# Performance work log

Hardware: AMD Instinct MI355X
Metric: run time of the kernel (lower is better)

## Reference

```python
import jax, jax.numpy as jnp
import numpy as np

MAX_DISP = 24  # matches init_kwargs


def setup_inputs() -> dict:
    key = jax.random.key(0)
    k1, k2 = jax.random.split(key)
    B, H, W, C = 2, 256, 256, 16
    left = jax.random.normal(k1, (B, H, W, C), dtype=jnp.float32)
    right = jax.random.normal(k2, (B, H, W, C), dtype=jnp.float32)
    return {"left": left, "right": right}


def reference(left, right):
    # left/right: [B, H, W, C]. Builds concat cost volume [B, 2*max_disp, H, W, 2C].
    # For disparity i in [-max_disp, max_disp): out[d, :, w] pairs left[w] with
    # right[w - i]; positions where w - i falls outside [0, W) are zero-padded
    # (both the left and right halves, matching tf.pad of the concatenated slice).
    W = left.shape[2]
    disps = jnp.arange(-MAX_DISP, MAX_DISP)              # [2D]
    idx = jnp.arange(W)[None, :] - disps[:, None]        # [2D, W] source col in right
    valid = (idx >= 0) & (idx < W)                       # [2D, W]
    idx_c = jnp.clip(idx, 0, W - 1)
    mask = valid[None, None, :, :, None].astype(left.dtype)  # [1,1,2D,W,1]
    r = right[:, :, idx_c, :] * mask                     # [B,H,2D,W,C]
    l = left[:, :, None, :, :] * mask                    # [B,H,2D,W,C]
    vol = jnp.concatenate([l, r], axis=-1)               # [B,H,2D,W,2C]
    return jnp.transpose(vol, (0, 2, 1, 3, 4))           # [B,2D,H,W,2C]
```

## Files before the change

kernel.cpp:

```cpp
#include <hip/hip_runtime.h>


#define MAXD 24
#define ND   48
#define HH   256
#define WW   256

__global__ __launch_bounds__(1024) void FeatureVolume_68762426409246_kernel(
    const float4* __restrict__ left,
    const float4* __restrict__ right,
    float4* __restrict__ out) {
    __shared__ float4 lds[2 * WW * 4];

    const unsigned int bh  = blockIdx.x;
    const unsigned int b   = bh >> 8;
    const unsigned int tid = threadIdx.x;

    const unsigned int row_base = bh * (WW * 4);
    lds[tid]          = left [row_base + tid];
    lds[WW * 4 + tid] = right[row_base + tid];
    __syncthreads();

    const unsigned int out_base = (b * (ND * HH) + (bh & 255u)) * (WW * 8);

    const unsigned int total = ND * WW * 8;
    for (unsigned int idx = tid; idx < total; idx += 1024) {
        unsigned int c4 = idx & 7u;
        unsigned int w  = (idx >> 3) & 255u;
        unsigned int d  = idx >> 11;

        int src_w  = (int)w - ((int)d - MAXD);
        bool valid = ((unsigned)src_w < (unsigned)WW);

        int col_r = min(max(src_w, 0), WW - 1);
        unsigned int col  = (c4 < 4u) ? w : (unsigned)col_r;
        unsigned int half = (c4 < 4u) ? 0u : (unsigned)(WW * 4);

        float4 v = lds[half + col * 4u + (c4 & 3u)];
        float  m = valid ? 1.0f : 0.0f;

        out[out_base + d * (HH * WW * 8) + (idx & 2047u)] =
            make_float4(v.x * m, v.y * m, v.z * m, v.w * m);
    }
}

extern "C" void kernel_launch(void* const* d_in, const int* in_sizes, int n_in,
                              void* d_out, int out_size, void* d_ws, size_t ws_size,
                              hipStream_t stream) {
    const float4* left  = (const float4*)d_in[0];
    const float4* right = (const float4*)d_in[1];
    float4* out = (float4*)d_out;

    FeatureVolume_68762426409246_kernel<<<2 * HH, 1024, 0, stream>>>(
        left, right, out);
}
```

Measured before the change: 152.4 us.

## Scatter each input float4 to all disparity slices instead of gathering via LDS

```diff
diff --git a/kernel.cpp b/kernel.cpp
--- a/kernel.cpp
+++ b/kernel.cpp
@@ -5,42 +5,45 @@
 #define ND   48
 #define HH   256
 #define WW   256
+#define SLICE_F4 (HH * WW * 8)
 
-__global__ __launch_bounds__(1024) void FeatureVolume_68762426409246_kernel(
+__global__ __launch_bounds__(256) void FeatureVolume_68762426409246_kernel(
     const float4* __restrict__ left,
     const float4* __restrict__ right,
     float4* __restrict__ out) {
-    __shared__ float4 lds[2 * WW * 4];
+    const unsigned int g = blockIdx.x * 256u + threadIdx.x;
 
-    const unsigned int bh  = blockIdx.x;
-    const unsigned int b   = bh >> 8;
-    const unsigned int tid = threadIdx.x;
+    const float4 L = left[g];
+    const float4 R = right[g];
 
-    const unsigned int row_base = bh * (WW * 4);
-    lds[tid]          = left [row_base + tid];
-    lds[WW * 4 + tid] = right[row_base + tid];
-    __syncthreads();
+    const unsigned int c4q = g & 3u;
+    const unsigned int w   = (g >> 2) & 255u;
+    const unsigned int h   = (g >> 10) & 255u;
+    const unsigned int b   = g >> 18;
 
-    const unsigned int out_base = (b * (ND * HH) + (bh & 255u)) * (WW * 8);
+    unsigned long long baseA =
+        (unsigned long long)(b * ND) * SLICE_F4 +
+        (unsigned long long)((h * WW + w) * 8u + c4q);
+    float4* pA = out + baseA;
+    float4* pC = pA + (-(int)MAXD * 8 + 4);
 
-    const unsigned int total = ND * WW * 8;
-    for (unsigned int idx = tid; idx < total; idx += 1024) {
-        unsigned int c4 = idx & 7u;
-        unsigned int w  = (idx >> 3) & 255u;
-        unsigned int d  = idx >> 11;
+    const float4 Z = make_float4(0.f, 0.f, 0.f, 0.f);
 
-        int src_w  = (int)w - ((int)d - MAXD);
-        bool valid = ((unsigned)src_w < (unsigned)WW);
+    int vA = (int)w + MAXD;
+    int vC = (int)w - MAXD;
 
-        int col_r = min(max(src_w, 0), WW - 1);
-        unsigned int col  = (c4 < 4u) ? w : (unsigned)col_r;
-        unsigned int half = (c4 < 4u) ? 0u : (unsigned)(WW * 4);
+    #pragma unroll 4
+    for (int d = 0; d < ND; ++d) {
+        const bool valid = ((unsigned int)vA < (unsigned int)WW);
 
-        float4 v = lds[half + col * 4u + (c4 & 3u)];
-        float  m = valid ? 1.0f : 0.0f;
+        pA[0] = valid ? L : Z;
+        if (!valid) pA[4] = Z;
+        if ((unsigned int)vC < (unsigned int)WW) pC[0] = R;
 
-        out[out_base + d * (HH * WW * 8) + (idx & 2047u)] =
-            make_float4(v.x * m, v.y * m, v.z * m, v.w * m);
+        pA += SLICE_F4;
+        pC += SLICE_F4 + 8;
+        vA -= 1;
+        vC += 1;
     }
 }
 
@@ -51,6 +54,6 @@
     const float4* right = (const float4*)d_in[1];
     float4* out = (float4*)d_out;
 
-    FeatureVolume_68762426409246_kernel<<<2 * HH, 1024, 0, stream>>>(
+    FeatureVolume_68762426409246_kernel<<<2048, 256, 0, stream>>>(
         left, right, out);
 }
```

Measured after the change: 275.4 us. 80.6% more time.

## Keep left features in registers and batch four disparities per loop iteration

Applied to the files above, without the earlier changes.

```diff
diff --git a/kernel.cpp b/kernel.cpp
--- a/kernel.cpp
+++ b/kernel.cpp
@@ -5,42 +5,54 @@
 #define ND   48
 #define HH   256
 #define WW   256
+#define SLICE 524288u
 
 __global__ __launch_bounds__(1024) void FeatureVolume_68762426409246_kernel(
     const float4* __restrict__ left,
     const float4* __restrict__ right,
     float4* __restrict__ out) {
-    __shared__ float4 lds[2 * WW * 4];
+    __shared__ float4 rlds[WW * 4];
 
     const unsigned int bh  = blockIdx.x;
     const unsigned int b   = bh >> 8;
-    const unsigned int tid = threadIdx.x;
+    const unsigned int t   = threadIdx.x;
+    const unsigned int c4  = t & 7u;
+    const unsigned int wlo = t >> 3;
+    const unsigned int row = bh << 10;
 
-    const unsigned int row_base = bh * (WW * 4);
-    lds[tid]          = left [row_base + tid];
-    lds[WW * 4 + tid] = right[row_base + tid];
+    rlds[t] = right[row + t];
+
+    const unsigned int lbase = row + (wlo << 2) + (c4 & 3u);
+    const float4 L0 = left[lbase];
+    const float4 L1 = left[lbase + 512u];
     __syncthreads();
 
-    const unsigned int out_base = (b * (ND * HH) + (bh & 255u)) * (WW * 8);
+    const bool   isL = (c4 < 4u);
+    const float4 Z   = make_float4(0.f, 0.f, 0.f, 0.f);
 
-    const unsigned int total = ND * WW * 8;
-    for (unsigned int idx = tid; idx < total; idx += 1024) {
-        unsigned int c4 = idx & 7u;
-        unsigned int w  = (idx >> 3) & 255u;
-        unsigned int d  = idx >> 11;
+    float4* o0 = out + (((unsigned long long)(b * ND * HH + (bh & 255u))) << 11) + t;
 
-        int src_w  = (int)w - ((int)d - MAXD);
-        bool valid = ((unsigned)src_w < (unsigned)WW);
-
-        int col_r = min(max(src_w, 0), WW - 1);
-        unsigned int col  = (c4 < 4u) ? w : (unsigned)col_r;
-        unsigned int half = (c4 < 4u) ? 0u : (unsigned)(WW * 4);
-
-        float4 v = lds[half + col * 4u + (c4 & 3u)];
-        float  m = valid ? 1.0f : 0.0f;
-
-        out[out_base + d * (HH * WW * 8) + (idx & 2047u)] =
-            make_float4(v.x * m, v.y * m, v.z * m, v.w * m);
+    for (int d = 0; d < ND; d += 4) {
+        float4 v[4][2];
+        #pragma unroll
+        for (int k = 0; k < 4; ++k) {
+            const int s0 = (int)wlo + MAXD - (d + k);
+            const int s1 = s0 + 128;
+            const int c0 = min(max(s0, 0), WW - 1);
+            const int c1 = min(max(s1, 0), WW - 1);
+            const float4 r0 = rlds[(c0 << 2) + (int)(c4 & 3u)];
+            const float4 r1 = rlds[(c1 << 2) + (int)(c4 & 3u)];
+            const float4 a0 = isL ? L0 : r0;
+            const float4 a1 = isL ? L1 : r1;
+            v[k][0] = ((unsigned)s0 < (unsigned)WW) ? a0 : Z;
+            v[k][1] = ((unsigned)s1 < (unsigned)WW) ? a1 : Z;
+        }
+        #pragma unroll
+        for (int k = 0; k < 4; ++k) {
+            float4* p = o0 + (unsigned)(d + k) * SLICE;
+            p[0]    = v[k][0];
+            p[1024] = v[k][1];
+        }
     }
 }
 
```

Result: slower. 479.1 us (+214.3%).

## Split work by disparity and row chunk with double-buffered LDS row prefetch

Applied to the files above, without the earlier changes.

```diff
diff --git a/kernel.cpp b/kernel.cpp
--- a/kernel.cpp
+++ b/kernel.cpp
@@ -5,42 +5,72 @@
 #define ND   48
 #define HH   256
 #define WW   256
+#define HC   16
+#define ROW_F4 1024
+#define OUT_ROW_F4 2048
+#define SLICE_F4 (HH * OUT_ROW_F4)
 
 __global__ __launch_bounds__(1024) void FeatureVolume_68762426409246_kernel(
     const float4* __restrict__ left,
     const float4* __restrict__ right,
     float4* __restrict__ out) {
-    __shared__ float4 lds[2 * WW * 4];
+    __shared__ float4 buf[2][2 * ROW_F4];
 
-    const unsigned int bh  = blockIdx.x;
-    const unsigned int b   = bh >> 8;
-    const unsigned int tid = threadIdx.x;
+    const unsigned bid = blockIdx.x;
+    const unsigned hc  = bid & 15u;
+    const unsigned bd  = bid >> 4;
+    const unsigned b   = (bd >= ND) ? 1u : 0u;
+    const unsigned d   = bd - b * ND;
+    const unsigned t   = threadIdx.x;
 
-    const unsigned int row_base = bh * (WW * 4);
-    lds[tid]          = left [row_base + tid];
-    lds[WW * 4 + tid] = right[row_base + tid];
+    const unsigned h0 = hc * HC;
+    const float4* lrow = left  + (size_t)(b * HH + h0) * ROW_F4;
+    const float4* rrow = right + (size_t)(b * HH + h0) * ROW_F4;
+
+    {
+        float4 lv = lrow[t];
+        float4 rv = rrow[t];
+        buf[0][t]          = lv;
+        buf[0][ROW_F4 + t] = rv;
+    }
     __syncthreads();
 
-    const unsigned int out_base = (b * (ND * HH) + (bh & 255u)) * (WW * 8);
+    const unsigned c4 = t & 7u;
+    const unsigned w  = t >> 3;
+    const bool isL = (c4 < 4u);
+    const int s0 = (int)w + MAXD - (int)d;
+    const int s1 = s0 + 128;
+    const bool val0 = ((unsigned)s0 < (unsigned)WW);
+    const bool val1 = ((unsigned)s1 < (unsigned)WW);
+    const unsigned cr0 = (unsigned)min(max(s0, 0), WW - 1);
+    const unsigned cr1 = (unsigned)min(max(s1, 0), WW - 1);
+    const unsigned a0 = isL ? (w * 4u + c4)
+                            : (ROW_F4 + cr0 * 4u + (c4 - 4u));
+    const unsigned a1 = isL ? ((w + 128u) * 4u + c4)
+                            : (ROW_F4 + cr1 * 4u + (c4 - 4u));
+    const float4 Z = make_float4(0.f, 0.f, 0.f, 0.f);
 
-    const unsigned int total = ND * WW * 8;
-    for (unsigned int idx = tid; idx < total; idx += 1024) {
-        unsigned int c4 = idx & 7u;
-        unsigned int w  = (idx >> 3) & 255u;
-        unsigned int d  = idx >> 11;
+    float4* op = out + (size_t)bd * SLICE_F4 + (size_t)h0 * OUT_ROW_F4 + t;
 
-        int src_w  = (int)w - ((int)d - MAXD);
-        bool valid = ((unsigned)src_w < (unsigned)WW);
-
-        int col_r = min(max(src_w, 0), WW - 1);
-        unsigned int col  = (c4 < 4u) ? w : (unsigned)col_r;
-        unsigned int half = (c4 < 4u) ? 0u : (unsigned)(WW * 4);
-
-        float4 v = lds[half + col * 4u + (c4 & 3u)];
-        float  m = valid ? 1.0f : 0.0f;
-
-        out[out_base + d * (HH * WW * 8) + (idx & 2047u)] =
-            make_float4(v.x * m, v.y * m, v.z * m, v.w * m);
+    unsigned pp = 0;
+    for (int i = 0; i < HC; ++i) {
+        float4 lv, rv;
+        const bool more = (i + 1 < HC);
+        if (more) {
+            lv = lrow[(size_t)(i + 1) * ROW_F4 + t];
+            rv = rrow[(size_t)(i + 1) * ROW_F4 + t];
+        }
+        float4 x0 = buf[pp][a0];
+        float4 x1 = buf[pp][a1];
+        op[0]    = val0 ? x0 : Z;
+        op[1024] = val1 ? x1 : Z;
+        if (more) {
+            buf[pp ^ 1][t]          = lv;
+            buf[pp ^ 1][ROW_F4 + t] = rv;
+        }
+        __syncthreads();
+        pp ^= 1;
+        op += OUT_ROW_F4;
     }
 }
 
@@ -51,6 +81,6 @@
     const float4* right = (const float4*)d_in[1];
     float4* out = (float4*)d_out;
 
-    FeatureVolume_68762426409246_kernel<<<2 * HH, 1024, 0, stream>>>(
+    FeatureVolume_68762426409246_kernel<<<2 * ND * (HH / HC), 1024, 0, stream>>>(
         left, right, out);
 }
```

New measurement: 363.6 us. 2.39x slower.
